# Kernel optimization log

Hardware: AMD Instinct MI355X
Metric: run time of the kernel (lower is better)

The kernel has to match this reference:

```python
import jax, jax.numpy as jnp
import numpy as np

V = 4096   # vocal_size
M = 4      # markov_order
B = 8
L = 2048


def setup_inputs() -> dict:
    key = jax.random.key(0)
    k1, k2 = jax.random.split(key, 2)
    idx = jax.random.randint(k1, (B, L), 0, V, dtype=jnp.int64 if jax.config.jax_enable_x64 else jnp.int32)
    fan_in = M * (V + 1)
    # nn.Linear default init: U(-1/sqrt(fan_in), 1/sqrt(fan_in))
    bound = 1.0 / np.sqrt(fan_in)
    W = jax.random.uniform(k2, (V, fan_in), minval=-bound, maxval=bound, dtype=jnp.float32)
    b = jax.random.uniform(jax.random.fold_in(k2, 1), (V,), minval=-bound, maxval=bound, dtype=jnp.float32)
    return {"idx": idx, "W": W, "b": b}


def _contexts(idx, vocab, order):
    # Reproduces the roll-and-pad loop: x[..., k] = idx shifted right by (order-1-k),
    # with the first (order-1-k) positions filled with the pad token `vocab`.
    Bb, Ll = idx.shape
    cols = []
    for k in range(order):
        s = order - 1 - k
        if s == 0:
            cols.append(idx)
        else:
            pad = jnp.full((Bb, s), vocab, dtype=idx.dtype)
            cols.append(jnp.concatenate([pad, idx[:, : Ll - s]], axis=1))
    return jnp.stack(cols, axis=-1)  # [B, L, M]


def reference(idx, W, b):
    vocab = W.shape[0]
    order = W.shape[1] // (vocab + 1)
    x = _contexts(idx, vocab, order)          # [B, L, M]
    # one_hot(x) @ W.T == gather rows of W.T per table; split W.T into M tables.
    Wt = W.T.reshape(order, vocab + 1, vocab)  # [M, V+1, V]
    logits = b
    for k in range(order):  # small fixed loop over markov order
        logits = logits + Wt[k][x[..., k]]     # [B, L, V]
    return logits
```

## Files before the change

kernel.cpp:

```cpp
#include <hip/hip_runtime.h>
#include <hip/hip_bf16.h>
#include <cstdint>

#define VOCAB 4096
#define ORDER 4
#define FAN   16388
#define NL    2048
#define NPOS  16384
#define NCT   129

typedef float        f4 __attribute__((ext_vector_type(4)));
typedef unsigned int u4 __attribute__((ext_vector_type(4)));
typedef unsigned int u2 __attribute__((ext_vector_type(2)));

static __device__ __forceinline__ unsigned short f2bf(float f)
{
    __hip_bfloat16 h = __float2bfloat16(f);
    unsigned short r;
    __builtin_memcpy(&r, &h, 2);
    return r;
}

__global__ __launch_bounds__(512) void k_transpose_pipe(
    const float* __restrict__ W, unsigned short* __restrict__ Wt)
{
    extern __shared__ float buf[];

    const int b   = blockIdx.x;
    const int vt  = b & 31;
    const int g   = b >> 5;
    const int ct0 = (g * NCT) / 8;
    const int ct1 = ((g + 1) * NCT) / 8;
    const int v0  = vt * 128;

    const int tid  = threadIdx.x;
    const int lane = tid & 63;
    const int w    = tid >> 6;

    const int lrow_half = lane >> 5;
    const int lgran     = lane & 31;

    const int pth = (tid & 15) * 8;
    const int cb  = tid >> 4;
    const int sth = (tid & 15) & 7;

    int cur = 0;

    auto stage = [&](int ct, int pg) {
        const int c0 = ct * 128;
        #pragma unroll
        for (int i = 0; i < 8; ++i) {
            const int r = w * 16 + 2 * i + lrow_half;
            const int s = (r >> 3) & 7;
            int c = c0 + 4 * (lgran ^ s);
            if (c + 4 > FAN) c = c0;
            const float* gp = W + (size_t)(v0 + r) * FAN + c;
            float* lp = buf + pg * 16384 + (w * 16 + 2 * i) * 128;
            __builtin_amdgcn_global_load_lds(
                (const __attribute__((address_space(1))) unsigned int*)gp,
                (__attribute__((address_space(3))) unsigned int*)lp,
                16, 0, 2 );
        }
    };

    auto store_phase = [&](int ct, int pg) {
        const int c0 = ct * 128;
        const float* bp = buf + pg * 16384;
        #pragma unroll
        for (int i = 0; i < 4; ++i) {
            const int cl = cb + 32 * i;
            const int c  = c0 + cl;
            if (c < FAN) {
                const int gsw = (((cl >> 2) ^ sth) << 2) + (cl & 3);
                unsigned short sv[8];
                #pragma unroll
                for (int j = 0; j < 8; ++j)
                    sv[j] = f2bf(bp[(pth + j) * 128 + gsw]);
                u4 pk;
                pk.x = (unsigned)sv[0] | ((unsigned)sv[1] << 16);
                pk.y = (unsigned)sv[2] | ((unsigned)sv[3] << 16);
                pk.z = (unsigned)sv[4] | ((unsigned)sv[5] << 16);
                pk.w = (unsigned)sv[6] | ((unsigned)sv[7] << 16);
                *(u4*)(Wt + (size_t)c * VOCAB + v0 + pth) = pk;
            }
        }
    };

    stage(ct0, 0);
    __syncthreads();

    for (int t = ct0; t < ct1; ++t) {
        const bool more = (t + 1 < ct1);
        if (more) stage(t + 1, cur ^ 1);
        store_phase(t, cur);
        if (more) {
            asm volatile("s_waitcnt vmcnt(4)" ::: "memory");
            __builtin_amdgcn_s_barrier();
        }
        cur ^= 1;
    }
}

__global__ __launch_bounds__(512) void k_transpose_bf16(
    const float* __restrict__ W, unsigned short* __restrict__ Wt)
{
    __shared__ float tile[128][129];
    const int c0 = blockIdx.x * 128;
    const int v0 = blockIdx.y * 128;

    const int cq = (threadIdx.x & 31) * 4;
    const int vr = threadIdx.x >> 5;
    const bool cvalid = (c0 + cq) < FAN;

    #pragma unroll
    for (int i = 0; i < 8; ++i) {
        const int v = vr + 16 * i;
        if (cvalid) {
            const f4 f = __builtin_nontemporal_load(
                (const f4*)(W + (size_t)(v0 + v) * FAN + (c0 + cq)));
            tile[v][cq + 0] = f.x;
            tile[v][cq + 1] = f.y;
            tile[v][cq + 2] = f.z;
            tile[v][cq + 3] = f.w;
        }
    }
    __syncthreads();

    const int p  = (threadIdx.x & 15) * 8;
    const int cb = threadIdx.x >> 4;

    #pragma unroll
    for (int i = 0; i < 4; ++i) {
        const int cl = cb + 32 * i;
        const int c  = c0 + cl;
        if (c < FAN) {
            unsigned short s[8];
            #pragma unroll
            for (int j = 0; j < 8; ++j)
                s[j] = f2bf(tile[p + j][cl]);
            u4 pk;
            pk.x = (unsigned)s[0] | ((unsigned)s[1] << 16);
            pk.y = (unsigned)s[2] | ((unsigned)s[3] << 16);
            pk.z = (unsigned)s[4] | ((unsigned)s[5] << 16);
            pk.w = (unsigned)s[6] | ((unsigned)s[7] << 16);
            *(u4*)(Wt + (size_t)c * VOCAB + v0 + p) = pk;
        }
    }
}

__global__ __launch_bounds__(256) void k_gather4(
    const int* __restrict__ idx, const unsigned short* __restrict__ Wt,
    const float* __restrict__ bias, float* __restrict__ out)
{
    const int pp = blockIdx.x * 4;
    const int bb = pp >> 11;
    const int l0 = pp & (NL - 1);
    const int* row = idx + bb * NL;

    unsigned off[4][ORDER];
    #pragma unroll
    for (int p = 0; p < 4; ++p) {
        #pragma unroll
        for (int k = 0; k < ORDER; ++k) {
            const int s   = ORDER - 1 - k;
            const int lp  = l0 + p;
            const int tok = (lp >= s) ? row[lp - s] : VOCAB;
            off[p][k] = (unsigned)(((size_t)(k * (VOCAB + 1) + tok) * VOCAB) * 2u);
        }
    }

    const char* Wb = (const char*)Wt;
    float* o = out + (size_t)pp * VOCAB;
    const int j4 = threadIdx.x * 4;

    #pragma unroll
    for (int seg = 0; seg < 4; ++seg) {
        const int v    = seg * 1024 + j4;
        const int voff = v * 2;

        const f4 bv = *(const f4*)(bias + v);

        u2 wv[4][ORDER];
        #pragma unroll
        for (int p = 0; p < 4; ++p)
            #pragma unroll
            for (int k = 0; k < ORDER; ++k)
                wv[p][k] = *(const u2*)(Wb + off[p][k] + voff);

        #pragma unroll
        for (int p = 0; p < 4; ++p) {
            float a0 = bv.x, a1 = bv.y, a2 = bv.z, a3 = bv.w;
            #pragma unroll
            for (int k = 0; k < ORDER; ++k) {
                const unsigned lo = wv[p][k].x, hi = wv[p][k].y;
                a0 += __uint_as_float(lo << 16);
                a1 += __uint_as_float(lo & 0xFFFF0000u);
                a2 += __uint_as_float(hi << 16);
                a3 += __uint_as_float(hi & 0xFFFF0000u);
            }
            f4 sv; sv.x = a0; sv.y = a1; sv.z = a2; sv.w = a3;
            __builtin_nontemporal_store(sv, (f4*)(o + (size_t)p * VOCAB + v));
        }
    }
}

__global__ __launch_bounds__(256) void k_direct(
    const int* __restrict__ idx, const float* __restrict__ W,
    const float* __restrict__ bias, float* __restrict__ out)
{
    const int pos = blockIdx.x;
    const int bb  = pos >> 11;
    const int ll  = pos & (NL - 1);
    const int* row = idx + bb * NL;

    int off[ORDER];
    #pragma unroll
    for (int k = 0; k < ORDER; ++k) {
        const int s   = ORDER - 1 - k;
        const int tok = (ll >= s) ? row[ll - s] : VOCAB;
        off[k] = k * (VOCAB + 1) + tok;
    }

    float* o = out + (size_t)pos * VOCAB;
    for (int v = threadIdx.x; v < VOCAB; v += 256) {
        const float* wr = W + (size_t)v * FAN;
        o[v] = bias[v] + wr[off[0]] + wr[off[1]] + wr[off[2]] + wr[off[3]];
    }
}

extern "C" void kernel_launch(void* const* d_in, const int* in_sizes, int n_in,
                              void* d_out, int out_size, void* d_ws, size_t ws_size,
                              hipStream_t stream)
{
    const int*   idx  = (const int*)d_in[0];
    const float* W    = (const float*)d_in[1];
    const float* bias = (const float*)d_in[2];
    float*       out  = (float*)d_out;

    const size_t wt_bytes = (size_t)FAN * VOCAB * 2;

    if (ws_size >= wt_bytes) {
        unsigned short* Wt = (unsigned short*)d_ws;

        static int pipe_ok = -1;
        if (pipe_ok < 0) {
            pipe_ok = (hipFuncSetAttribute(
                           (const void*)k_transpose_pipe,
                           hipFuncAttributeMaxDynamicSharedMemorySize,
                           131072) == hipSuccess) ? 1 : 0;
        }

        if (pipe_ok) {
            k_transpose_pipe<<<256, 512, 131072, stream>>>(W, Wt);
        } else {
            dim3 g1((FAN + 127) / 128, VOCAB / 128);
            k_transpose_bf16<<<g1, 512, 0, stream>>>(W, Wt);
        }
        k_gather4<<<NPOS / 4, 256, 0, stream>>>(idx, Wt, bias, out);
    } else {
        k_direct<<<NPOS, 256, 0, stream>>>(idx, W, bias, out);
    }
}
```

Measured before the change: 513.8 us.

## Fuse transpose and gather into one cooperative kernel with grid sync

Replaces the separate pipelined transpose kernel and gather kernel with a single cooperative kernel of 512 blocks. Each block first transposes a contiguous range of 128x128 tiles of W into a bf16 workspace through a padded LDS tile, then all blocks meet at a grid-wide sync and run the gather-sum for 32 positions each. The aim is to remove the second kernel launch and its gap. In exchange it drops the async global-to-LDS double-buffered pipeline, adds the cost of a grid barrier, and is limited to a grid that must be fully co-resident.

```diff
diff --git a/kernel.cpp b/kernel.cpp
--- a/kernel.cpp
+++ b/kernel.cpp
@@ -1,6 +1,9 @@
 #include <hip/hip_runtime.h>
 #include <hip/hip_bf16.h>
+#include <hip/hip_cooperative_groups.h>
 #include <cstdint>
+
+namespace cg = cooperative_groups;
 
 #define VOCAB 4096
 #define ORDER 4
@@ -8,6 +11,10 @@
 #define NL    2048
 #define NPOS  16384
 #define NCT   129
+#define NVT   32
+#define NTILE 4128
+#define NBLK  512
+#define TILE_LDS (128 * 129 * 4)
 
 typedef float        f4 __attribute__((ext_vector_type(4)));
 typedef unsigned int u4 __attribute__((ext_vector_type(4)));
@@ -21,83 +28,126 @@
     return r;
 }
 
-__global__ __launch_bounds__(512) void k_transpose_pipe(
-    const float* __restrict__ W, unsigned short* __restrict__ Wt)
-{
-    extern __shared__ float buf[];
-
+__global__ __launch_bounds__(256) void k_fused(
+    const int* __restrict__ idx, const float* __restrict__ W,
+    const float* __restrict__ bias, float* __restrict__ out,
+    unsigned short* __restrict__ Wt)
+{
+    extern __shared__ float tile[];
     const int b   = blockIdx.x;
-    const int vt  = b & 31;
-    const int g   = b >> 5;
-    const int ct0 = (g * NCT) / 8;
-    const int ct1 = ((g + 1) * NCT) / 8;
-    const int v0  = vt * 128;
-
-    const int tid  = threadIdx.x;
-    const int lane = tid & 63;
-    const int w    = tid >> 6;
-
-    const int lrow_half = lane >> 5;
-    const int lgran     = lane & 31;
-
-    const int pth = (tid & 15) * 8;
-    const int cb  = tid >> 4;
-    const int sth = (tid & 15) & 7;
-
-    int cur = 0;
-
-    auto stage = [&](int ct, int pg) {
-        const int c0 = ct * 128;
+    const int tid = threadIdx.x;
+
+    {
+        const int t0 = (b * NTILE) / NBLK;
+        const int t1 = ((b + 1) * NTILE) / NBLK;
+
+        const int cq  = (tid & 31) * 4;
+        const int vr  = tid >> 5;
+        const int pth = (tid & 15) * 8;
+        const int cb  = tid >> 4;
+
+        for (int t = t0; t < t1; ++t) {
+            const int vt = t / NCT;
+            const int ct = t - vt * NCT;
+            const int v0 = vt * 128;
+            const int c0 = ct * 128;
+            const bool cvalid = (c0 + cq) < FAN;
+
+            #pragma unroll
+            for (int i = 0; i < 16; ++i) {
+                const int v = vr + 8 * i;
+                if (cvalid) {
+                    const f4 f = __builtin_nontemporal_load(
+                        (const f4*)(W + (size_t)(v0 + v) * FAN + (c0 + cq)));
+                    tile[v * 129 + cq + 0] = f.x;
+                    tile[v * 129 + cq + 1] = f.y;
+                    tile[v * 129 + cq + 2] = f.z;
+                    tile[v * 129 + cq + 3] = f.w;
+                }
+            }
+            __syncthreads();
+
+            #pragma unroll
+            for (int i = 0; i < 8; ++i) {
+                const int cl = cb + 16 * i;
+                const int c  = c0 + cl;
+                if (c < FAN) {
+                    unsigned short s[8];
+                    #pragma unroll
+                    for (int j = 0; j < 8; ++j)
+                        s[j] = f2bf(tile[(pth + j) * 129 + cl]);
+                    u4 pk;
+                    pk.x = (unsigned)s[0] | ((unsigned)s[1] << 16);
+                    pk.y = (unsigned)s[2] | ((unsigned)s[3] << 16);
+                    pk.z = (unsigned)s[4] | ((unsigned)s[5] << 16);
+                    pk.w = (unsigned)s[6] | ((unsigned)s[7] << 16);
+                    *(u4*)(Wt + (size_t)c * VOCAB + v0 + pth) = pk;
+                }
+            }
+            __syncthreads();
+        }
+    }
+
+    cg::this_grid().sync();
+
+    {
+        const int j4 = tid * 4;
+
+        f4 bv[4];
         #pragma unroll
-        for (int i = 0; i < 8; ++i) {
-            const int r = w * 16 + 2 * i + lrow_half;
-            const int s = (r >> 3) & 7;
-            int c = c0 + 4 * (lgran ^ s);
-            if (c + 4 > FAN) c = c0;
-            const float* gp = W + (size_t)(v0 + r) * FAN + c;
-            float* lp = buf + pg * 16384 + (w * 16 + 2 * i) * 128;
-            __builtin_amdgcn_global_load_lds(
-                (const __attribute__((address_space(1))) unsigned int*)gp,
-                (__attribute__((address_space(3))) unsigned int*)lp,
-                16, 0, 2 );
-        }
-    };
-
-    auto store_phase = [&](int ct, int pg) {
-        const int c0 = ct * 128;
-        const float* bp = buf + pg * 16384;
-        #pragma unroll
-        for (int i = 0; i < 4; ++i) {
-            const int cl = cb + 32 * i;
-            const int c  = c0 + cl;
-            if (c < FAN) {
-                const int gsw = (((cl >> 2) ^ sth) << 2) + (cl & 3);
-                unsigned short sv[8];
+        for (int s = 0; s < 4; ++s)
+            bv[s] = *(const f4*)(bias + s * 1024 + j4);
+
+        const int bb   = b >> 6;
+        const int lba  = (b * 32) & (NL - 1);
+        const int* row = idx + bb * NL;
+        const char* Wb = (const char*)Wt;
+
+        for (int gi = 0; gi < 8; ++gi) {
+            const int l0 = lba + gi * 4;
+            unsigned off[4][ORDER];
+            #pragma unroll
+            for (int p = 0; p < 4; ++p) {
                 #pragma unroll
-                for (int j = 0; j < 8; ++j)
-                    sv[j] = f2bf(bp[(pth + j) * 128 + gsw]);
-                u4 pk;
-                pk.x = (unsigned)sv[0] | ((unsigned)sv[1] << 16);
-                pk.y = (unsigned)sv[2] | ((unsigned)sv[3] << 16);
-                pk.z = (unsigned)sv[4] | ((unsigned)sv[5] << 16);
-                pk.w = (unsigned)sv[6] | ((unsigned)sv[7] << 16);
-                *(u4*)(Wt + (size_t)c * VOCAB + v0 + pth) = pk;
-            }
-        }
-    };
-
-    stage(ct0, 0);
-    __syncthreads();
-
-    for (int t = ct0; t < ct1; ++t) {
-        const bool more = (t + 1 < ct1);
-        if (more) stage(t + 1, cur ^ 1);
-        store_phase(t, cur);
-        if (more) {
-            asm volatile("s_waitcnt vmcnt(4)" ::: "memory");
-            __builtin_amdgcn_s_barrier();
-        }
-        cur ^= 1;
+                for (int k = 0; k < ORDER; ++k) {
+                    const int s   = ORDER - 1 - k;
+                    const int lp  = l0 + p;
+                    const int tok = (lp >= s) ? row[lp - s] : VOCAB;
+                    off[p][k] = (unsigned)(((size_t)(k * (VOCAB + 1) + tok) * VOCAB) * 2u);
+                }
+            }
+
+            float* o = out + ((size_t)bb * NL + l0) * VOCAB;
+
+            #pragma unroll
+            for (int seg = 0; seg < 4; ++seg) {
+                const int v    = seg * 1024 + j4;
+                const int voff = v * 2;
+
+                u2 wv[4][ORDER];
+                #pragma unroll
+                for (int p = 0; p < 4; ++p)
+                    #pragma unroll
+                    for (int k = 0; k < ORDER; ++k)
+                        wv[p][k] = *(const u2*)(Wb + off[p][k] + voff);
+
+                #pragma unroll
+                for (int p = 0; p < 4; ++p) {
+                    float a0 = bv[seg].x, a1 = bv[seg].y,
+                          a2 = bv[seg].z, a3 = bv[seg].w;
+                    #pragma unroll
+                    for (int k = 0; k < ORDER; ++k) {
+                        const unsigned lo = wv[p][k].x, hi = wv[p][k].y;
+                        a0 += __uint_as_float(lo << 16);
+                        a1 += __uint_as_float(lo & 0xFFFF0000u);
+                        a2 += __uint_as_float(hi << 16);
+                        a3 += __uint_as_float(hi & 0xFFFF0000u);
+                    }
+                    f4 sv; sv.x = a0; sv.y = a1; sv.z = a2; sv.w = a3;
+                    __builtin_nontemporal_store(sv, (f4*)(o + (size_t)p * VOCAB + v));
+                }
+            }
+        }
     }
 }
 
@@ -177,8 +227,7 @@
     for (int seg = 0; seg < 4; ++seg) {
         const int v    = seg * 1024 + j4;
         const int voff = v * 2;
-
-        const f4 bv = *(const f4*)(bias + v);
+        const f4 bvv = *(const f4*)(bias + v);
 
         u2 wv[4][ORDER];
         #pragma unroll
@@ -189,7 +238,7 @@
 
         #pragma unroll
         for (int p = 0; p < 4; ++p) {
-            float a0 = bv.x, a1 = bv.y, a2 = bv.z, a3 = bv.w;
+            float a0 = bvv.x, a1 = bvv.y, a2 = bvv.z, a3 = bvv.w;
             #pragma unroll
             for (int k = 0; k < ORDER; ++k) {
                 const unsigned lo = wv[p][k].x, hi = wv[p][k].y;
@@ -242,21 +291,33 @@
     if (ws_size >= wt_bytes) {
         unsigned short* Wt = (unsigned short*)d_ws;
 
-        static int pipe_ok = -1;
-        if (pipe_ok < 0) {
-            pipe_ok = (hipFuncSetAttribute(
-                           (const void*)k_transpose_pipe,
-                           hipFuncAttributeMaxDynamicSharedMemorySize,
-                           131072) == hipSuccess) ? 1 : 0;
-        }
-
-        if (pipe_ok) {
-            k_transpose_pipe<<<256, 512, 131072, stream>>>(W, Wt);
-        } else {
+        static int coop_ok = -1;
+        if (coop_ok < 0) {
+            int dev = 0;
+            hipGetDevice(&dev);
+            int sup = 0;
+            hipDeviceGetAttribute(&sup, hipDeviceAttributeCooperativeLaunch, dev);
+            const hipError_t ea = hipFuncSetAttribute(
+                (const void*)k_fused,
+                hipFuncAttributeMaxDynamicSharedMemorySize, TILE_LDS);
+            coop_ok = (sup && ea == hipSuccess) ? 1 : 0;
+        }
+
+        bool done = false;
+        if (coop_ok) {
+            void* args[] = {(void*)&idx, (void*)&W, (void*)&bias,
+                            (void*)&out, (void*)&Wt};
+            const hipError_t e = hipLaunchCooperativeKernel(
+                (const void*)k_fused, dim3(NBLK), dim3(256),
+                args, TILE_LDS, stream);
+            if (e == hipSuccess) done = true; else coop_ok = 0;
+        }
+
+        if (!done) {
             dim3 g1((FAN + 127) / 128, VOCAB / 128);
             k_transpose_bf16<<<g1, 512, 0, stream>>>(W, Wt);
-        }
-        k_gather4<<<NPOS / 4, 256, 0, stream>>>(idx, Wt, bias, out);
+            k_gather4<<<NPOS / 4, 256, 0, stream>>>(idx, Wt, bias, out);
+        }
     } else {
         k_direct<<<NPOS, 256, 0, stream>>>(idx, W, bias, out);
     }
```

After: 598.3 us. 1.16x slower.
